# Optimization experiments

Hardware: AMD Instinct MI355X
Metric: run time of the kernel (lower is better)

## Reference

```python
import jax, jax.numpy as jnp
import numpy as np

N, LQ, D_MODEL, M_HEADS, P_POINTS, H_DIM, W_DIM = 8, 4096, 256, 8, 4, 64, 64


def setup_inputs() -> dict:
    key = jax.random.key(0)
    ks = jax.random.split(key, 9)
    d = D_MODEL
    scale = 1.0 / np.sqrt(d).astype(np.float32)
    return {
        "query": jax.random.normal(ks[0], (N, LQ, d), jnp.float32),
        "reference_points": jax.random.uniform(ks[1], (N, LQ, 2), jnp.float32),
        "input_flatten": jax.random.normal(ks[2], (N, H_DIM * W_DIM, d), jnp.float32),
        "H": H_DIM,
        "W": W_DIM,
        "Wv": jax.random.normal(ks[3], (d, d), jnp.float32) * scale,
        "bv": jnp.zeros((d,), jnp.float32),
        "Woff": jax.random.normal(ks[4], (M_HEADS * P_POINTS * 2, d), jnp.float32) * 0.01,
        "boff": jax.random.normal(ks[5], (M_HEADS * P_POINTS * 2,), jnp.float32) * 0.5,
        "Wa": jax.random.normal(ks[6], (M_HEADS * P_POINTS, d), jnp.float32) * 0.01,
        "ba": jnp.zeros((M_HEADS * P_POINTS,), jnp.float32),
        "Wo": jax.random.normal(ks[7], (d, d), jnp.float32) * scale,
        "bo": jnp.zeros((d,), jnp.float32),
    }


def _bilinear_sample(val, grid, H, W):
    # val: [B, D, H*W]; grid: [B, Lq, P, 2] in [-1, 1] (x, y); align_corners=False, zero padding.
    B, D, _ = val.shape
    _, Lq, P, _ = grid.shape
    x = (grid[..., 0] + 1.0) * (W * 0.5) - 0.5
    y = (grid[..., 1] + 1.0) * (H * 0.5) - 0.5
    x0 = jnp.floor(x)
    y0 = jnp.floor(y)
    x0i = x0.astype(jnp.int32)
    y0i = y0.astype(jnp.int32)
    wx1 = x - x0
    wy1 = y - y0
    out = jnp.zeros((B, D, Lq, P), val.dtype)
    for xi, wx in ((x0i, 1.0 - wx1), (x0i + 1, wx1)):
        for yi, wy in ((y0i, 1.0 - wy1), (y0i + 1, wy1)):
            valid = (xi >= 0) & (xi < W) & (yi >= 0) & (yi < H)
            idx = jnp.clip(yi, 0, H - 1) * W + jnp.clip(xi, 0, W - 1)  # [B, Lq, P]
            g = jnp.take_along_axis(val, idx.reshape(B, 1, Lq * P), axis=2).reshape(B, D, Lq, P)
            w = jnp.where(valid, wx * wy, 0.0)
            out = out + g * w[:, None]
    return out


def reference(query, reference_points, input_flatten, H, W, Wv, bv, Woff, boff, Wa, ba, Wo, bo):
    n, lq, d = query.shape
    m, p = M_HEADS, P_POINTS
    dh = d // m
    value = (input_flatten @ Wv.T + bv).reshape(n, H * W, m, dh)
    offsets = (query @ Woff.T + boff).reshape(n, lq, m, p, 2)
    attw = jax.nn.softmax((query @ Wa.T + ba).reshape(n, lq, m, p), axis=-1)
    normalizer = jnp.array([W, H], dtype=query.dtype)  # [W, H] order per torch code
    loc = reference_points[:, :, None, None, :] + offsets / normalizer
    grid = 2.0 * loc - 1.0  # [n, lq, m, p, 2]
    # value -> [n*m, dh, H*W] matching torch flatten(2).transpose(1,2).reshape
    val = jnp.transpose(value, (0, 2, 3, 1)).reshape(n * m, dh, H * W)
    grd = jnp.transpose(grid, (0, 2, 1, 3, 4)).reshape(n * m, lq, p, 2)
    samp = _bilinear_sample(val, grd, H, W)  # [n*m, dh, lq, p]
    aw = jnp.transpose(attw, (0, 2, 1, 3)).reshape(n * m, 1, lq, p)
    out = (samp * aw).sum(-1).reshape(n, m * dh, lq)
    out = jnp.transpose(out, (0, 2, 1))  # [n, lq, d]
    return out @ Wo.T + bo
```

## Files before the change

kernel.cpp:

```cpp
#include <hip/hip_runtime.h>
#include <math.h>

#define NB   8
#define LQN  4096
#define DM   256
#define MH   8
#define PP   4
#define HH   64
#define WW   64
#define LG   128
#define PW   67
#define PPIX (PW*PW)

typedef __bf16 bf16x8 __attribute__((ext_vector_type(8)));
typedef float  f32x4  __attribute__((ext_vector_type(4)));
typedef unsigned short us8 __attribute__((ext_vector_type(8)));
typedef unsigned short us4 __attribute__((ext_vector_type(4)));

__device__ __forceinline__ unsigned short f2bf(float f) {
    unsigned u = __float_as_uint(f);
    u += 0x7FFFu + ((u >> 16) & 1u);
    return (unsigned short)(u >> 16);
}
__device__ __forceinline__ unsigned short bfb(float v) {
    __bf16 b = (__bf16)v;
    return __builtin_bit_cast(unsigned short, b);
}
__device__ __forceinline__ float bf2f(unsigned short b) {
    return __uint_as_float((unsigned)b << 16);
}

__device__ __forceinline__ void gl2lds16(const void* g, unsigned short* l) {
    __builtin_amdgcn_global_load_lds(
        (const __attribute__((address_space(1))) void*)g,
        (__attribute__((address_space(3))) void*)l,
        16, 0, 0);
}

__global__ __launch_bounds__(256, 2)
void dual_gemm(const float* __restrict__ Ain, const float* __restrict__ Aq,
               const unsigned short* __restrict__ Wvh,
               const unsigned short* __restrict__ Wcath,
               const float* __restrict__ bv, const float* __restrict__ bcat,
               unsigned short* __restrict__ valueP,
               unsigned short* __restrict__ logitsB) {
    constexpr int K = 256, NK = 8;
    __shared__ unsigned short sA[2][8192];
    __shared__ unsigned short sB[2][4096];

    const int t    = threadIdx.x;
    const int blk  = blockIdx.x;
    const bool isVal = (blk < 512);

    const float* A; const unsigned short* B; const float* bias;
    int brow, bcol;
    if (isVal) { A = Ain; B = Wvh;   bias = bv;
                 brow = (blk >> 1) * 128; bcol = (blk & 1) * 128; }
    else       { A = Aq;  B = Wcath; bias = bcat;
                 brow = (blk - 512) * 128; bcol = 0; }

    const int arow = t >> 3;
    const int acsw = (t & 7) ^ (arow & 7);
    const float* aG = A + (size_t)(brow + arow) * K + acsw * 4;
    const size_t aIss = (size_t)32 * K;

    const unsigned short* bG = B + (size_t)(bcol + (t >> 2)) * K + (t & 3) * 8;
    const size_t brs64 = (size_t)64 * K;

    const int l   = t & 63;
    const int wid = t >> 6;
    const int wr  = wid >> 1, wc = wid & 1;
    const int fr  = l & 15,   kq = l >> 4;

    f32x4 acc[4][4] = {};

#define STAGE(buf, ks_) { const int k0_ = (ks_) * 32;                    \
       gl2lds16(aG + k0_,            &sA[buf][t * 8]);                   \
       gl2lds16(aG + k0_ + aIss,     &sA[buf][2048 + t * 8]);            \
       gl2lds16(aG + k0_ + 2 * aIss, &sA[buf][4096 + t * 8]);            \
       gl2lds16(aG + k0_ + 3 * aIss, &sA[buf][6144 + t * 8]);            \
       gl2lds16(bG + k0_,            &sB[buf][t * 8]);                   \
       gl2lds16(bG + k0_ + brs64,    &sB[buf][2048 + t * 8]); }

    STAGE(0, 0);
    STAGE(1, 1);

    const int fr7 = fr & 7;
    for (int ks = 0; ks < NK; ++ks) {
        const int cur = ks & 1;
        if (ks < NK - 1) asm volatile("s_waitcnt vmcnt(6)" ::: "memory");
        else             asm volatile("s_waitcnt vmcnt(0)" ::: "memory");
        __builtin_amdgcn_s_barrier();
        __builtin_amdgcn_sched_barrier(0);

        bf16x8 af[4], bf_[4];
#pragma unroll
        for (int m = 0; m < 4; ++m) {
            const int row = wr * 64 + m * 16 + fr;
            const int u0  = row * 8 + ((kq * 2) ^ fr7);
            const int u1  = u0 ^ 1;
            const f32x4 a0 = *(const f32x4*)&sA[cur][u0 * 8];
            const f32x4 a1 = *(const f32x4*)&sA[cur][u1 * 8];
            bf16x8 v;
            v[0] = (__bf16)a0[0]; v[1] = (__bf16)a0[1];
            v[2] = (__bf16)a0[2]; v[3] = (__bf16)a0[3];
            v[4] = (__bf16)a1[0]; v[5] = (__bf16)a1[1];
            v[6] = (__bf16)a1[2]; v[7] = (__bf16)a1[3];
            af[m] = v;
        }
#pragma unroll
        for (int n = 0; n < 4; ++n)
            bf_[n] = *(const bf16x8*)&sB[cur][(wc * 64 + n * 16 + fr) * 32 + kq * 8];

#pragma unroll
        for (int m = 0; m < 4; ++m)
#pragma unroll
            for (int n = 0; n < 4; ++n)
                acc[m][n] = __builtin_amdgcn_mfma_f32_16x16x32_bf16(
                    bf_[n], af[m], acc[m][n], 0, 0, 0);

        __builtin_amdgcn_sched_barrier(0);
        __builtin_amdgcn_s_barrier();
        if (ks + 2 < NK) STAGE(cur, ks + 2);
    }
#undef STAGE

#pragma unroll
    for (int m = 0; m < 4; ++m) {
        const int row = brow + wr * 64 + m * 16 + fr;
        size_t rbase;
        if (isVal) {
            const int nb_ = row >> 12;
            const int pix = row & 4095;
            const int y   = pix >> 6, x = pix & 63;
            rbase = ((size_t)nb_ * PPIX + (size_t)(y + 1) * PW + (x + 1)) * DM;
        } else {
            rbase = (size_t)row * LG;
        }
#pragma unroll
        for (int n = 0; n < 4; ++n) {
            const int colq = bcol + wc * 64 + n * 16 + kq * 4;
            const float4 bs = *(const float4*)&bias[colq];
            us4 o;
            o[0] = bfb(acc[m][n][0] + bs.x);
            o[1] = bfb(acc[m][n][1] + bs.y);
            o[2] = bfb(acc[m][n][2] + bs.z);
            o[3] = bfb(acc[m][n][3] + bs.w);
            *(us4*)&(isVal ? valueP : logitsB)[rbase + colq] = o;
        }
    }
}

__global__ __launch_bounds__(256, 2)
void gemm_out(const unsigned short* __restrict__ A,
              const unsigned short* __restrict__ B,
              const float* __restrict__ bias, float* __restrict__ C) {
    constexpr int K = 256, N = DM, NK = 8;
    __shared__ unsigned short sA[2][4096];
    __shared__ unsigned short sB[2][4096];

    const int t    = threadIdx.x;
    const int bx   = (blockIdx.x & 7) * 32 + (blockIdx.x >> 3);
    const int brow = bx * 128;
    const int bcol = blockIdx.y * 128;

    const unsigned short* aG = A + (size_t)(brow + (t >> 2)) * K + (t & 3) * 8;
    const unsigned short* bG = B + (size_t)(bcol + (t >> 2)) * K + (t & 3) * 8;
    const size_t rs64 = (size_t)64 * K;

    const int l   = t & 63;
    const int wid = t >> 6;
    const int wr  = wid >> 1, wc = wid & 1;
    const int fr  = l & 15,   kq = l >> 4;

    f32x4 acc[4][4] = {};

#define STAGEO(buf, ks_) { const int k0_ = (ks_) * 32;                   \
       gl2lds16(aG + k0_,        &sA[buf][t * 8]);                       \
       gl2lds16(aG + k0_ + rs64, &sA[buf][2048 + t * 8]);                \
       gl2lds16(bG + k0_,        &sB[buf][t * 8]);                       \
       gl2lds16(bG + k0_ + rs64, &sB[buf][2048 + t * 8]); }

    STAGEO(0, 0);
    STAGEO(1, 1);

    for (int ks = 0; ks < NK; ++ks) {
        const int cur = ks & 1;
        if (ks < NK - 1) asm volatile("s_waitcnt vmcnt(4)" ::: "memory");
        else             asm volatile("s_waitcnt vmcnt(0)" ::: "memory");
        __builtin_amdgcn_s_barrier();
        __builtin_amdgcn_sched_barrier(0);

        bf16x8 af[4], bfr[4];
#pragma unroll
        for (int m = 0; m < 4; ++m)
            af[m]  = *(const bf16x8*)&sA[cur][(wr * 64 + m * 16 + fr) * 32 + kq * 8];
#pragma unroll
        for (int n = 0; n < 4; ++n)
            bfr[n] = *(const bf16x8*)&sB[cur][(wc * 64 + n * 16 + fr) * 32 + kq * 8];
#pragma unroll
        for (int m = 0; m < 4; ++m)
#pragma unroll
            for (int n = 0; n < 4; ++n)
                acc[m][n] = __builtin_amdgcn_mfma_f32_16x16x32_bf16(
                    bfr[n], af[m], acc[m][n], 0, 0, 0);

        __builtin_amdgcn_sched_barrier(0);
        __builtin_amdgcn_s_barrier();
        if (ks + 2 < NK) STAGEO(cur, ks + 2);
    }
#undef STAGEO

#pragma unroll
    for (int m = 0; m < 4; ++m) {
        const int row = brow + wr * 64 + m * 16 + fr;
#pragma unroll
        for (int n = 0; n < 4; ++n) {
            const int colq = bcol + wc * 64 + n * 16 + kq * 4;
            const float4 bs = *(const float4*)&bias[colq];
            float4 o;
            o.x = acc[m][n][0] + bs.x; o.y = acc[m][n][1] + bs.y;
            o.z = acc[m][n][2] + bs.z; o.w = acc[m][n][3] + bs.w;
            *(float4*)&C[(size_t)row * N + colq] = o;
        }
    }
}

__global__ __launch_bounds__(256)
void prep_kernel(const float* __restrict__ Wv, const float* __restrict__ Wo,
                 const float* __restrict__ Woff, const float* __restrict__ Wa,
                 const float* __restrict__ boff, const float* __restrict__ ba,
                 unsigned short* __restrict__ Wvh, unsigned short* __restrict__ Woh,
                 unsigned short* __restrict__ Wcath, float* __restrict__ bcat,
                 unsigned short* __restrict__ valueP) {
    const int i = blockIdx.x * 256 + threadIdx.x;
    if (i < 65536) {
        Wvh[i] = f2bf(Wv[i]);
    } else if (i < 131072) {
        const int j = i - 65536;
        Woh[j] = f2bf(Wo[j]);
    } else if (i < 163840) {
        const int j = i - 131072, n = j >> 8, k = j & 255;
        const float v = (n < 64) ? Woff[n * 256 + k]
                                 : ((n < 96) ? Wa[(n - 64) * 256 + k] : 0.f);
        Wcath[j] = f2bf(v);
    } else if (i < 163968) {
        const int n = i - 163840;
        bcat[n] = (n < 64) ? boff[n] : ((n < 96) ? ba[n - 64] : 0.f);
    } else if (i < 163968 + 201216) {
        const int j   = i - 163968;
        const int c4  = j & 63;
        const int pix = j >> 6;
        const int n   = pix / 393;
        const int r   = pix - n * 393;
        int x, y;
        if (r < 201) {
            const int q = r / 67;
            y = (q == 0) ? 0 : (q == 1 ? 65 : 66);
            x = r - q * 67;
        } else {
            const int q = r - 201;
            y = 1 + q / 3;
            const int s = q - (q / 3) * 3;
            x = (s == 0) ? 0 : (s == 1 ? 65 : 66);
        }
        const size_t addr = ((size_t)n * PPIX + (size_t)y * PW + x) * DM + c4 * 4;
        *(ushort4*)&valueP[addr] = make_ushort4(0, 0, 0, 0);
    }
}

__global__ __launch_bounds__(256)
void sample_kernel(const float* __restrict__ refp,
                   const unsigned short* __restrict__ valueP,
                   const unsigned short* __restrict__ logitsB,
                   unsigned short* __restrict__ sampledH) {
    const int vb   = (blockIdx.x & 7) * 1024 + (blockIdx.x >> 3);
    const int wid  = threadIdx.x >> 6;
    const int b    = vb * 4 + wid;
    const int n    = b >> 12;
    const int lane = threadIdx.x & 63;

    const int tp  = lane & 31;
    const int pm  = tp >> 2, ppt = tp & 3;
    const unsigned short* lg = logitsB + (size_t)b * LG;

    const float rx = refp[(size_t)b * 2 + 0];
    const float ry = refp[(size_t)b * 2 + 1];
    const float ox = bf2f(lg[pm * 8 + ppt * 2 + 0]);
    const float oy = bf2f(lg[pm * 8 + ppt * 2 + 1]);
    const float la = bf2f(lg[64 + tp]);

    const float x = fminf(fmaxf(fmaf(rx, (float)WW, ox) - 0.5f, -1.0f), 64.0f);
    const float y = fminf(fmaxf(fmaf(ry, (float)HH, oy) - 0.5f, -1.0f), 64.0f);

    float mx = fmaxf(la, __shfl_xor(la, 1));
    mx = fmaxf(mx, __shfl_xor(mx, 2));
    const float e = __expf(la - mx);
    float den = e + __shfl_xor(e, 1);
    den += __shfl_xor(den, 2);
    const float w = e / den;

    const int half = lane >> 5;
    const int c8   = lane & 31;
    const int mh   = c8 >> 2;
    const unsigned short* vbase = valueP + (size_t)n * (PPIX * DM) + c8 * 8;

    float accv[8] = {};
#pragma unroll
    for (int p = 0; p < PP; ++p) {
        const int   sl = mh * PP + p;
        const float xp = __shfl(x, sl);
        const float yp = __shfl(y, sl);
        const float wp = __shfl(w, sl);

        const float x0f = floorf(xp), y0f = floorf(yp);
        const int   x0 = (int)x0f,   y0 = (int)y0f;
        const float wx1 = xp - x0f,  wy1 = yp - y0f;
        const float wy  = half ? wy1 : (1.f - wy1);
        const float wA  = wp * wy * (1.f - wx1);
        const float wB  = wp * wy * wx1;

        const unsigned short* p0 =
            vbase + (size_t)((y0 + 1 + half) * PW + (x0 + 1)) * DM;
        const us8 gA = *(const us8*)(p0);
        const us8 gB = *(const us8*)(p0 + DM);
#pragma unroll
        for (int j = 0; j < 8; ++j) {
            accv[j] = fmaf(wA, bf2f(gA[j]), accv[j]);
            accv[j] = fmaf(wB, bf2f(gB[j]), accv[j]);
        }
    }

#pragma unroll
    for (int j = 0; j < 8; ++j)
        accv[j] += __shfl_xor(accv[j], 32);

    if (half == 0) {
        us8 o;
#pragma unroll
        for (int j = 0; j < 8; ++j) o[j] = f2bf(accv[j]);
        *(us8*)&sampledH[(size_t)b * DM + c8 * 8] = o;
    }
}

extern "C" void kernel_launch(void* const* d_in, const int* in_sizes, int n_in,
                              void* d_out, int out_size, void* d_ws, size_t ws_size,
                              hipStream_t stream) {
    const float* query  = (const float*)d_in[0];
    const float* refp   = (const float*)d_in[1];
    const float* inputf = (const float*)d_in[2];
    const float* Wv   = (const float*)d_in[5];
    const float* bv   = (const float*)d_in[6];
    const float* Woff = (const float*)d_in[7];
    const float* boff = (const float*)d_in[8];
    const float* Wa   = (const float*)d_in[9];
    const float* ba   = (const float*)d_in[10];
    const float* Wo   = (const float*)d_in[11];
    const float* bo   = (const float*)d_in[12];
    float* out = (float*)d_out;

    const int Mrows = NB * LQN;

    unsigned short* sampledH = (unsigned short*)d_ws;
    unsigned short* valueP   = sampledH + (size_t)Mrows * DM;
    unsigned short* logitsB  = valueP   + (size_t)NB * PPIX * DM;
    unsigned short* Wvh      = logitsB  + (size_t)Mrows * LG;
    unsigned short* Woh      = Wvh      + 65536;
    unsigned short* Wcath    = Woh      + 65536;
    float*          bcat     = (float*)(Wcath + 32768);

    prep_kernel<<<1427, 256, 0, stream>>>(Wv, Wo, Woff, Wa, boff, ba,
                                          Wvh, Woh, Wcath, bcat, valueP);

    dual_gemm<<<768, 256, 0, stream>>>(inputf, query, Wvh, Wcath, bv, bcat,
                                       valueP, logitsB);

    sample_kernel<<<Mrows / 4, 256, 0, stream>>>(refp, valueP, logitsB, sampledH);

    {
        dim3 g(Mrows / 128, DM / 128);
        gemm_out<<<g, 256, 0, stream>>>(sampledH, Woh, bo, out);
    }
}
```

Baseline: 64.55 us.

## Drop prep kernel: load fp32 weights directly and convert in GEMM LDS path

Removes the separate prep kernel that converted weights to bf16 and zeroed the padded border. Both GEMMs now stream fp32 weights into LDS and convert them to bf16 while building fragments, and the border zeroing moves into the tail of dual_gemm. Block indices are remapped so that groups of row tiles share a column tile, which should improve L2 reuse. This saves a kernel launch and a pass over the weights, but doubles the LDS traffic and the conversion work for the B operand inside the GEMM inner loops.

```diff
diff --git a/kernel.cpp b/kernel.cpp
--- a/kernel.cpp
+++ b/kernel.cpp
@@ -22,10 +22,6 @@
     u += 0x7FFFu + ((u >> 16) & 1u);
     return (unsigned short)(u >> 16);
 }
-__device__ __forceinline__ unsigned short bfb(float v) {
-    __bf16 b = (__bf16)v;
-    return __builtin_bit_cast(unsigned short, b);
-}
 __device__ __forceinline__ float bf2f(unsigned short b) {
     return __uint_as_float((unsigned)b << 16);
 }
@@ -37,35 +33,62 @@
         16, 0, 0);
 }
 
+__device__ __forceinline__ bf16x8 cvt_frag(const unsigned short* s, int row, int kq) {
+    const int u0 = row * 8 + ((kq * 2) ^ (row & 7));
+    const int u1 = u0 ^ 1;
+    const f32x4 a0 = *(const f32x4*)&s[u0 * 8];
+    const f32x4 a1 = *(const f32x4*)&s[u1 * 8];
+    bf16x8 v;
+    v[0] = (__bf16)a0[0]; v[1] = (__bf16)a0[1];
+    v[2] = (__bf16)a0[2]; v[3] = (__bf16)a0[3];
+    v[4] = (__bf16)a1[0]; v[5] = (__bf16)a1[1];
+    v[6] = (__bf16)a1[2]; v[7] = (__bf16)a1[3];
+    return v;
+}
+
 __global__ __launch_bounds__(256, 2)
 void dual_gemm(const float* __restrict__ Ain, const float* __restrict__ Aq,
-               const unsigned short* __restrict__ Wvh,
-               const unsigned short* __restrict__ Wcath,
-               const float* __restrict__ bv, const float* __restrict__ bcat,
+               const float* __restrict__ Wv,  const float* __restrict__ Woff,
+               const float* __restrict__ Wa,  const float* __restrict__ bv,
+               const float* __restrict__ boff, const float* __restrict__ ba,
                unsigned short* __restrict__ valueP,
                unsigned short* __restrict__ logitsB) {
     constexpr int K = 256, NK = 8;
     __shared__ unsigned short sA[2][8192];
-    __shared__ unsigned short sB[2][4096];
-
-    const int t    = threadIdx.x;
-    const int blk  = blockIdx.x;
+    __shared__ unsigned short sB[2][8192];
+
+    const int t   = threadIdx.x;
+    const int blk = blockIdx.x;
     const bool isVal = (blk < 512);
 
-    const float* A; const unsigned short* B; const float* bias;
+    const float* A;
     int brow, bcol;
-    if (isVal) { A = Ain; B = Wvh;   bias = bv;
-                 brow = (blk >> 1) * 128; bcol = (blk & 1) * 128; }
-    else       { A = Aq;  B = Wcath; bias = bcat;
-                 brow = (blk - 512) * 128; bcol = 0; }
-
-    const int arow = t >> 3;
-    const int acsw = (t & 7) ^ (arow & 7);
-    const float* aG = A + (size_t)(brow + arow) * K + acsw * 4;
+    if (isVal) {
+        const int g = blk >> 4, w = blk & 15;
+        brow = (g * 8 + (w & 7)) * 128;
+        bcol = ((w >> 3) & 1) * 128;
+        A = Ain;
+    } else {
+        brow = (blk - 512) * 128; bcol = 0; A = Aq;
+    }
+
+    const int srow = t >> 3;
+    const int scq  = (t & 7) ^ (srow & 7);
+    const float* aG = A + (size_t)(brow + srow) * K + scq * 4;
     const size_t aIss = (size_t)32 * K;
 
-    const unsigned short* bG = B + (size_t)(bcol + (t >> 2)) * K + (t & 3) * 8;
-    const size_t brs64 = (size_t)64 * K;
+    const float *bS0, *bS1, *bS2, *bS3;
+    if (isVal) {
+        bS0 = Wv + (size_t)(bcol +  0 + srow) * K + scq * 4;
+        bS1 = Wv + (size_t)(bcol + 32 + srow) * K + scq * 4;
+        bS2 = Wv + (size_t)(bcol + 64 + srow) * K + scq * 4;
+        bS3 = Wv + (size_t)(bcol + 96 + srow) * K + scq * 4;
+    } else {
+        bS0 = Woff + (size_t)(srow)      * K + scq * 4;
+        bS1 = Woff + (size_t)(32 + srow) * K + scq * 4;
+        bS2 = Wa   + (size_t)(srow)      * K + scq * 4;
+        bS3 = Woff + (size_t)(srow)      * K + scq * 4;
+    }
 
     const int l   = t & 63;
     const int wid = t >> 6;
@@ -79,38 +102,28 @@
        gl2lds16(aG + k0_ + aIss,     &sA[buf][2048 + t * 8]);            \
        gl2lds16(aG + k0_ + 2 * aIss, &sA[buf][4096 + t * 8]);            \
        gl2lds16(aG + k0_ + 3 * aIss, &sA[buf][6144 + t * 8]);            \
-       gl2lds16(bG + k0_,            &sB[buf][t * 8]);                   \
-       gl2lds16(bG + k0_ + brs64,    &sB[buf][2048 + t * 8]); }
+       gl2lds16(bS0 + k0_,           &sB[buf][t * 8]);                   \
+       gl2lds16(bS1 + k0_,           &sB[buf][2048 + t * 8]);            \
+       gl2lds16(bS2 + k0_,           &sB[buf][4096 + t * 8]);            \
+       gl2lds16(bS3 + k0_,           &sB[buf][6144 + t * 8]); }
 
     STAGE(0, 0);
     STAGE(1, 1);
 
-    const int fr7 = fr & 7;
     for (int ks = 0; ks < NK; ++ks) {
         const int cur = ks & 1;
-        if (ks < NK - 1) asm volatile("s_waitcnt vmcnt(6)" ::: "memory");
+        if (ks < NK - 1) asm volatile("s_waitcnt vmcnt(8)" ::: "memory");
         else             asm volatile("s_waitcnt vmcnt(0)" ::: "memory");
         __builtin_amdgcn_s_barrier();
         __builtin_amdgcn_sched_barrier(0);
 
         bf16x8 af[4], bf_[4];
 #pragma unroll
-        for (int m = 0; m < 4; ++m) {
-            const int row = wr * 64 + m * 16 + fr;
-            const int u0  = row * 8 + ((kq * 2) ^ fr7);
-            const int u1  = u0 ^ 1;
-            const f32x4 a0 = *(const f32x4*)&sA[cur][u0 * 8];
-            const f32x4 a1 = *(const f32x4*)&sA[cur][u1 * 8];
-            bf16x8 v;
-            v[0] = (__bf16)a0[0]; v[1] = (__bf16)a0[1];
-            v[2] = (__bf16)a0[2]; v[3] = (__bf16)a0[3];
-            v[4] = (__bf16)a1[0]; v[5] = (__bf16)a1[1];
-            v[6] = (__bf16)a1[2]; v[7] = (__bf16)a1[3];
-            af[m] = v;
-        }
+        for (int m = 0; m < 4; ++m)
+            af[m]  = cvt_frag(sA[cur], wr * 64 + m * 16 + fr, kq);
 #pragma unroll
         for (int n = 0; n < 4; ++n)
-            bf_[n] = *(const bf16x8*)&sB[cur][(wc * 64 + n * 16 + fr) * 32 + kq * 8];
+            bf_[n] = cvt_frag(sB[cur], wc * 64 + n * 16 + fr, kq);
 
 #pragma unroll
         for (int m = 0; m < 4; ++m)
@@ -140,117 +153,24 @@
 #pragma unroll
         for (int n = 0; n < 4; ++n) {
             const int colq = bcol + wc * 64 + n * 16 + kq * 4;
-            const float4 bs = *(const float4*)&bias[colq];
+            float4 b4;
+            if (isVal)            b4 = *(const float4*)&bv[colq];
+            else if (colq < 64)   b4 = *(const float4*)&boff[colq];
+            else if (colq < 96)   b4 = *(const float4*)&ba[colq - 64];
+            else                  b4 = make_float4(0.f, 0.f, 0.f, 0.f);
             us4 o;
-            o[0] = bfb(acc[m][n][0] + bs.x);
-            o[1] = bfb(acc[m][n][1] + bs.y);
-            o[2] = bfb(acc[m][n][2] + bs.z);
-            o[3] = bfb(acc[m][n][3] + bs.w);
+            o[0] = f2bf(acc[m][n][0] + b4.x);
+            o[1] = f2bf(acc[m][n][1] + b4.y);
+            o[2] = f2bf(acc[m][n][2] + b4.z);
+            o[3] = f2bf(acc[m][n][3] + b4.w);
             *(us4*)&(isVal ? valueP : logitsB)[rbase + colq] = o;
         }
     }
-}
-
-__global__ __launch_bounds__(256, 2)
-void gemm_out(const unsigned short* __restrict__ A,
-              const unsigned short* __restrict__ B,
-              const float* __restrict__ bias, float* __restrict__ C) {
-    constexpr int K = 256, N = DM, NK = 8;
-    __shared__ unsigned short sA[2][4096];
-    __shared__ unsigned short sB[2][4096];
-
-    const int t    = threadIdx.x;
-    const int bx   = (blockIdx.x & 7) * 32 + (blockIdx.x >> 3);
-    const int brow = bx * 128;
-    const int bcol = blockIdx.y * 128;
-
-    const unsigned short* aG = A + (size_t)(brow + (t >> 2)) * K + (t & 3) * 8;
-    const unsigned short* bG = B + (size_t)(bcol + (t >> 2)) * K + (t & 3) * 8;
-    const size_t rs64 = (size_t)64 * K;
-
-    const int l   = t & 63;
-    const int wid = t >> 6;
-    const int wr  = wid >> 1, wc = wid & 1;
-    const int fr  = l & 15,   kq = l >> 4;
-
-    f32x4 acc[4][4] = {};
-
-#define STAGEO(buf, ks_) { const int k0_ = (ks_) * 32;                   \
-       gl2lds16(aG + k0_,        &sA[buf][t * 8]);                       \
-       gl2lds16(aG + k0_ + rs64, &sA[buf][2048 + t * 8]);                \
-       gl2lds16(bG + k0_,        &sB[buf][t * 8]);                       \
-       gl2lds16(bG + k0_ + rs64, &sB[buf][2048 + t * 8]); }
-
-    STAGEO(0, 0);
-    STAGEO(1, 1);
-
-    for (int ks = 0; ks < NK; ++ks) {
-        const int cur = ks & 1;
-        if (ks < NK - 1) asm volatile("s_waitcnt vmcnt(4)" ::: "memory");
-        else             asm volatile("s_waitcnt vmcnt(0)" ::: "memory");
-        __builtin_amdgcn_s_barrier();
-        __builtin_amdgcn_sched_barrier(0);
-
-        bf16x8 af[4], bfr[4];
-#pragma unroll
-        for (int m = 0; m < 4; ++m)
-            af[m]  = *(const bf16x8*)&sA[cur][(wr * 64 + m * 16 + fr) * 32 + kq * 8];
-#pragma unroll
-        for (int n = 0; n < 4; ++n)
-            bfr[n] = *(const bf16x8*)&sB[cur][(wc * 64 + n * 16 + fr) * 32 + kq * 8];
-#pragma unroll
-        for (int m = 0; m < 4; ++m)
-#pragma unroll
-            for (int n = 0; n < 4; ++n)
-                acc[m][n] = __builtin_amdgcn_mfma_f32_16x16x32_bf16(
-                    bfr[n], af[m], acc[m][n], 0, 0, 0);
-
-        __builtin_amdgcn_sched_barrier(0);
-        __builtin_amdgcn_s_barrier();
-        if (ks + 2 < NK) STAGEO(cur, ks + 2);
-    }
-#undef STAGEO
-
-#pragma unroll
-    for (int m = 0; m < 4; ++m) {
-        const int row = brow + wr * 64 + m * 16 + fr;
-#pragma unroll
-        for (int n = 0; n < 4; ++n) {
-            const int colq = bcol + wc * 64 + n * 16 + kq * 4;
-            const float4 bs = *(const float4*)&bias[colq];
-            float4 o;
-            o.x = acc[m][n][0] + bs.x; o.y = acc[m][n][1] + bs.y;
-            o.z = acc[m][n][2] + bs.z; o.w = acc[m][n][3] + bs.w;
-            *(float4*)&C[(size_t)row * N + colq] = o;
-        }
-    }
-}
-
-__global__ __launch_bounds__(256)
-void prep_kernel(const float* __restrict__ Wv, const float* __restrict__ Wo,
-                 const float* __restrict__ Woff, const float* __restrict__ Wa,
-                 const float* __restrict__ boff, const float* __restrict__ ba,
-                 unsigned short* __restrict__ Wvh, unsigned short* __restrict__ Woh,
-                 unsigned short* __restrict__ Wcath, float* __restrict__ bcat,
-                 unsigned short* __restrict__ valueP) {
-    const int i = blockIdx.x * 256 + threadIdx.x;
-    if (i < 65536) {
-        Wvh[i] = f2bf(Wv[i]);
-    } else if (i < 131072) {
-        const int j = i - 65536;
-        Woh[j] = f2bf(Wo[j]);
-    } else if (i < 163840) {
-        const int j = i - 131072, n = j >> 8, k = j & 255;
-        const float v = (n < 64) ? Woff[n * 256 + k]
-                                 : ((n < 96) ? Wa[(n - 64) * 256 + k] : 0.f);
-        Wcath[j] = f2bf(v);
-    } else if (i < 163968) {
-        const int n = i - 163840;
-        bcat[n] = (n < 64) ? boff[n] : ((n < 96) ? ba[n - 64] : 0.f);
-    } else if (i < 163968 + 201216) {
-        const int j   = i - 163968;
-        const int c4  = j & 63;
-        const int pix = j >> 6;
+
+    const int gtid = blk * 256 + t;
+    for (int i = gtid; i < 201216; i += 196608) {
+        const int c4  = i & 63;
+        const int pix = i >> 6;
         const int n   = pix / 393;
         const int r   = pix - n * 393;
         int x, y;
@@ -266,6 +186,91 @@
         }
         const size_t addr = ((size_t)n * PPIX + (size_t)y * PW + x) * DM + c4 * 4;
         *(ushort4*)&valueP[addr] = make_ushort4(0, 0, 0, 0);
+    }
+}
+
+__global__ __launch_bounds__(256, 2)
+void gemm_out(const unsigned short* __restrict__ A,
+              const float* __restrict__ Wo,
+              const float* __restrict__ bo, float* __restrict__ C) {
+    constexpr int K = 256, N = DM, NK = 8;
+    __shared__ unsigned short sA[2][4096];
+    __shared__ unsigned short sB[2][8192];
+
+    const int t   = threadIdx.x;
+    const int blk = blockIdx.x;
+    const int g = blk >> 4, w = blk & 15;
+    const int brow = (g * 8 + (w & 7)) * 128;
+    const int bcol = ((w >> 3) & 1) * 128;
+
+    const unsigned short* aG = A + (size_t)(brow + (t >> 2)) * K + (t & 3) * 8;
+    const size_t ars64 = (size_t)64 * K;
+
+    const int srow = t >> 3;
+    const int scq  = (t & 7) ^ (srow & 7);
+    const float* bS0 = Wo + (size_t)(bcol +  0 + srow) * K + scq * 4;
+    const float* bS1 = Wo + (size_t)(bcol + 32 + srow) * K + scq * 4;
+    const float* bS2 = Wo + (size_t)(bcol + 64 + srow) * K + scq * 4;
+    const float* bS3 = Wo + (size_t)(bcol + 96 + srow) * K + scq * 4;
+
+    const int l   = t & 63;
+    const int wid = t >> 6;
+    const int wr  = wid >> 1, wc = wid & 1;
+    const int fr  = l & 15,   kq = l >> 4;
+
+    f32x4 acc[4][4] = {};
+
+#define STAGEO(buf, ks_) { const int k0_ = (ks_) * 32;                   \
+       gl2lds16(aG + k0_,         &sA[buf][t * 8]);                      \
+       gl2lds16(aG + k0_ + ars64, &sA[buf][2048 + t * 8]);               \
+       gl2lds16(bS0 + k0_,        &sB[buf][t * 8]);                      \
+       gl2lds16(bS1 + k0_,        &sB[buf][2048 + t * 8]);               \
+       gl2lds16(bS2 + k0_,        &sB[buf][4096 + t * 8]);               \
+       gl2lds16(bS3 + k0_,        &sB[buf][6144 + t * 8]); }
+
+    STAGEO(0, 0);
+    STAGEO(1, 1);
+
+    for (int ks = 0; ks < NK; ++ks) {
+        const int cur = ks & 1;
+        if (ks < NK - 1) asm volatile("s_waitcnt vmcnt(6)" ::: "memory");
+        else             asm volatile("s_waitcnt vmcnt(0)" ::: "memory");
+        __builtin_amdgcn_s_barrier();
+        __builtin_amdgcn_sched_barrier(0);
+
+        bf16x8 af[4], bfr[4];
+#pragma unroll
+        for (int m = 0; m < 4; ++m)
+            af[m]  = *(const bf16x8*)&sA[cur][(wr * 64 + m * 16 + fr) * 32 + kq * 8];
+#pragma unroll
+        for (int n = 0; n < 4; ++n)
+            bfr[n] = cvt_frag(sB[cur], wc * 64 + n * 16 + fr, kq);
+
+#pragma unroll
+        for (int m = 0; m < 4; ++m)
+#pragma unroll
+            for (int n = 0; n < 4; ++n)
+                acc[m][n] = __builtin_amdgcn_mfma_f32_16x16x32_bf16(
+                    bfr[n], af[m], acc[m][n], 0, 0, 0);
+
+        __builtin_amdgcn_sched_barrier(0);
+        __builtin_amdgcn_s_barrier();
+        if (ks + 2 < NK) STAGEO(cur, ks + 2);
+    }
+#undef STAGEO
+
+#pragma unroll
+    for (int m = 0; m < 4; ++m) {
+        const int row = brow + wr * 64 + m * 16 + fr;
+#pragma unroll
+        for (int n = 0; n < 4; ++n) {
+            const int colq = bcol + wc * 64 + n * 16 + kq * 4;
+            const float4 bs = *(const float4*)&bo[colq];
+            float4 o;
+            o.x = acc[m][n][0] + bs.x; o.y = acc[m][n][1] + bs.y;
+            o.z = acc[m][n][2] + bs.z; o.w = acc[m][n][3] + bs.w;
+            *(float4*)&C[(size_t)row * N + colq] = o;
+        }
     }
 }
 
@@ -364,21 +369,11 @@
     unsigned short* sampledH = (unsigned short*)d_ws;
     unsigned short* valueP   = sampledH + (size_t)Mrows * DM;
     unsigned short* logitsB  = valueP   + (size_t)NB * PPIX * DM;
-    unsigned short* Wvh      = logitsB  + (size_t)Mrows * LG;
-    unsigned short* Woh      = Wvh      + 65536;
-    unsigned short* Wcath    = Woh      + 65536;
-    float*          bcat     = (float*)(Wcath + 32768);
-
-    prep_kernel<<<1427, 256, 0, stream>>>(Wv, Wo, Woff, Wa, boff, ba,
-                                          Wvh, Woh, Wcath, bcat, valueP);
-
-    dual_gemm<<<768, 256, 0, stream>>>(inputf, query, Wvh, Wcath, bv, bcat,
-                                       valueP, logitsB);
+
+    dual_gemm<<<768, 256, 0, stream>>>(inputf, query, Wv, Woff, Wa,
+                                       bv, boff, ba, valueP, logitsB);
 
     sample_kernel<<<Mrows / 4, 256, 0, stream>>>(refp, valueP, logitsB, sampledH);
 
-    {
-        dim3 g(Mrows / 128, DM / 128);
-        gemm_out<<<g, 256, 0, stream>>>(sampledH, Woh, bo, out);
-    }
-}
+    gemm_out<<<512, 256, 0, stream>>>(sampledH, Wo, bo, out);
+}
```

Measured after the change: 65.71 us. About the same (+1.8%).
